# Optimization experiments

Hardware: AMD Instinct MI355X
Metric: run time of the kernel (lower is better)

The kernel has to match this reference:

```python
import jax, jax.numpy as jnp
import numpy as np

B, S, H, NH = 2, 2048, 1024, 16
HD = H // NH


def setup_inputs() -> dict:
    key = jax.random.key(0)
    ks = jax.random.split(key, 14)
    lim = 1.0 / np.sqrt(H)  # torch Linear default init range
    def lin(ka, kb):
        W = jax.random.uniform(ka, (H, H), jnp.float32, -lim, lim)
        b = jax.random.uniform(kb, (H,), jnp.float32, -lim, lim)
        return W, b
    Wq, bq = lin(ks[0], ks[1])
    Wk, bk = lin(ks[2], ks[3])
    Wv, bv = lin(ks[4], ks[5])
    Wo, bo = lin(ks[6], ks[7])
    return {
        "query": jax.random.normal(ks[8], (B, S, H), jnp.float32),
        "key": jax.random.normal(ks[9], (B, S, H), jnp.float32),
        "value": jax.random.normal(ks[10], (B, S, H), jnp.float32),
        "attn_mask": jax.random.randint(ks[11], (B, S, S), 0, 2).astype(bool),
        "relative_time": jax.random.normal(ks[12], (B, 1, S, S), jnp.float32),
        "Wq": Wq, "bq": bq, "Wk": Wk, "bk": bk,
        "Wv": Wv, "bv": bv, "Wo": Wo, "bo": bo,
    }


def reference(query, key, value, attn_mask, relative_time,
              Wq, bq, Wk, bk, Wv, bv, Wo, bo):
    Bq, Sq, _ = query.shape
    Skv = key.shape[1]
    # projections (torch Linear: x @ W^T + b)
    Q = (query @ Wq.T + bq).reshape(Bq, Sq, NH, HD).transpose(0, 2, 1, 3)
    K = (key @ Wk.T + bk).reshape(Bq, Skv, NH, HD).transpose(0, 2, 1, 3)
    V = (value @ Wv.T + bv).reshape(Bq, Skv, NH, HD).transpose(0, 2, 1, 3)
    scale = HD ** (-0.5)
    # NOTE: bias added BEFORE scaling, matching the original (non-standard)
    scores = jnp.einsum("bhqd,bhkd->bhqk", Q, K)
    scores = (scores + relative_time) * scale
    scores = jnp.where(attn_mask[:, None, :, :], scores, -jnp.inf)
    attn = jax.nn.softmax(scores.astype(jnp.float32), axis=-1).astype(scores.dtype)
    attn = jnp.nan_to_num(attn, nan=0.0)
    # dropout is identity in eval mode (dropout_rate applied only when training)
    out = jnp.einsum("bhqk,bhkd->bhqd", attn, V)
    out = out.transpose(0, 2, 1, 3).reshape(Bq, Sq, H)
    return out @ Wo.T + bo
```

## Files before the change

### kernel.cpp

```cpp
#include <hip/hip_runtime.h>
#include <hip/hip_bf16.h>

constexpr int BATCH = 2, SEQ = 2048, HDIM = 1024, NHEADS = 16, HEADD = 64;
constexpr int MROWS = BATCH * SEQ;
constexpr float QSCALE = 0.18033688011112042f;

typedef short short8  __attribute__((ext_vector_type(8)));
typedef float f32x4   __attribute__((ext_vector_type(4)));
typedef float f32x16  __attribute__((ext_vector_type(16)));
typedef int   int4v   __attribute__((ext_vector_type(4)));
typedef unsigned short ushort4v __attribute__((ext_vector_type(4)));

static __device__ __forceinline__ short f2bf(float f) {
    __hip_bfloat16 h = __float2bfloat16(f);
    return *reinterpret_cast<short*>(&h);
}

static __device__ __forceinline__ int cvt_pk_bf16(float a, float b) {
    int r;
    asm("v_cvt_pk_bf16_f32 %0, %1, %2" : "=v"(r) : "v"(a), "v"(b));
    return r;
}

static __device__ __forceinline__ float bfbits2f(unsigned short u) {
    return __builtin_bit_cast(float, (unsigned int)u << 16);
}

static __device__ __forceinline__ void gload_lds16(const void* g, void* l) {
    __builtin_amdgcn_global_load_lds(
        (const __attribute__((address_space(1))) unsigned int*)g,
        (__attribute__((address_space(3))) unsigned int*)l, 16, 0, 0);
}

__global__ void cvt_all_kernel(const float* __restrict__ q, const float* __restrict__ k,
                               const float* __restrict__ v, const float* __restrict__ w0,
                               const float* __restrict__ w1, const float* __restrict__ w2,
                               const float* __restrict__ w3,
                               short* __restrict__ xq, short* __restrict__ xk,
                               short* __restrict__ xv, short* __restrict__ o0,
                               short* __restrict__ o1, short* __restrict__ o2,
                               short* __restrict__ o3, int n4x, int n4w) {
    int i = blockIdx.x * blockDim.x + threadIdx.x;
    const int stride = gridDim.x * blockDim.x;
    const int total = 3 * n4x + 4 * n4w;
    for (; i < total; i += stride) {
        const float* in; short* out; int j = i;
        if (j < 3 * n4x) {
            if (j >= 2 * n4x)      { in = v; out = xv; j -= 2 * n4x; }
            else if (j >= n4x)     { in = k; out = xk; j -= n4x; }
            else                   { in = q; out = xq; }
        } else {
            j -= 3 * n4x;
            if (j >= 3 * n4w)      { in = w3; out = o3; j -= 3 * n4w; }
            else if (j >= 2 * n4w) { in = w2; out = o2; j -= 2 * n4w; }
            else if (j >= n4w)     { in = w1; out = o1; j -= n4w; }
            else                   { in = w0; out = o0; }
        }
        const float4 val = reinterpret_cast<const float4*>(in)[j];
        short4 o;
        o.x = f2bf(val.x); o.y = f2bf(val.y); o.z = f2bf(val.z); o.w = f2bf(val.w);
        reinterpret_cast<short4*>(out)[j] = o;
    }
}

__global__ void detect_mask_kernel(const unsigned int* __restrict__ m, int* flag) {
    const int tid = threadIdx.x;
    int gt1 = 0, isf = 0;
    for (int i = 0; i < 4; ++i) {
        unsigned int wv = m[tid + 256 * i];
        if (wv > 1u) gt1 = 1;
        if (wv == 0x3F800000u) isf = 1;
    }
    __shared__ int s_gt1, s_isf;
    if (tid == 0) { s_gt1 = 0; s_isf = 0; }
    __syncthreads();
    if (gt1) atomicOr(&s_gt1, 1);
    if (isf) atomicOr(&s_isf, 1);
    __syncthreads();
    if (tid == 0) flag[0] = s_gt1 ? (s_isf ? 2 : 1) : 0;
}

__global__ void fuse_rel_kernel(const float* __restrict__ rel, const void* __restrict__ mask,
                                const int* __restrict__ flag, short* __restrict__ rT,
                                int nThr) {
    const int f = flag[0];
    int i = blockIdx.x * blockDim.x + threadIdx.x;
    const int stride = gridDim.x * blockDim.x;
    for (; i < nThr; i += stride) {
        const int q    = i & 2047;
        const int kv16 = (i >> 11) & 127;
        const int b    = i >> 18;
        const long base = ((long)(b * 2048 + q)) * 2048 + kv16 * 16;
        float4 rv[4];
        #pragma unroll
        for (int g = 0; g < 4; ++g)
            rv[g] = *reinterpret_cast<const float4*>(rel + base + 4 * g);
        bool mk[16];
        if (f == 1) {
            const unsigned int* mp = (const unsigned int*)((const unsigned char*)mask + base);
            #pragma unroll
            for (int wd = 0; wd < 4; ++wd) {
                const unsigned int mw = mp[wd];
                #pragma unroll
                for (int s = 0; s < 4; ++s) mk[wd * 4 + s] = ((mw >> (8 * s)) & 0xffu) != 0;
            }
        } else if (f == 0) {
            const int* mp = (const int*)mask + base;
            #pragma unroll
            for (int j = 0; j < 16; ++j) mk[j] = mp[j] != 0;
        } else {
            const float* mp = (const float*)mask + base;
            #pragma unroll
            for (int j = 0; j < 16; ++j) mk[j] = mp[j] != 0.0f;
        }
        const float* rp = reinterpret_cast<const float*>(&rv[0]);
        #pragma unroll
        for (int g = 0; g < 4; ++g) {
            short4 o;
            short* op = reinterpret_cast<short*>(&o);
            #pragma unroll
            for (int j = 0; j < 4; ++j) {
                const int idx = 4 * g + j;
                op[j] = f2bf(mk[idx] ? rp[idx] * QSCALE : -1e30f);
            }
            *reinterpret_cast<short4*>(rT + (((long)(b * 512 + kv16 * 4 + g)) * 2048 + q) * 4) = o;
        }
    }
}

template<int BN, typename EPI>
static __device__ __forceinline__
void gemm_core(const short* A, const short* Bw, int K, int m0, int n0, EPI epi) {
    constexpr int NFRAG = BN / 32;
    __shared__ short As[128 * 64];
    __shared__ short Bs[BN * 64];
    const int tid  = threadIdx.x;
    const int lane = tid & 63;
    const int w    = tid >> 6;
    const int lo   = lane & 15, hi = lane >> 4;
    const int wm   = w >> 1, wn = w & 1;

    f32x4 acc[4][NFRAG] = {};

    const int arow = tid >> 3;
    const int acol = (tid & 7) * 8;
    const long aBase = (long)(m0 + arow) * K + acol;
    const long bBase = (long)(n0 + arow) * K + acol;

    for (int k0 = 0; k0 < K; k0 += 64) {
        #pragma unroll
        for (int i = 0; i < 4; ++i)
            gload_lds16(A + aBase + (long)i * 32 * K + k0, (char*)As + i * 4096 + tid * 16);
        #pragma unroll
        for (int i = 0; i < NFRAG; ++i)
            gload_lds16(Bw + bBase + (long)i * 32 * K + k0, (char*)Bs + i * 4096 + tid * 16);
        __syncthreads();
        #pragma unroll
        for (int ks = 0; ks < 2; ++ks) {
            short8 af[4], bf[NFRAG];
            const int koff = ks * 32 + hi * 8;
            #pragma unroll
            for (int fm = 0; fm < 4; ++fm)
                af[fm] = *reinterpret_cast<const short8*>(&As[(wm * 64 + fm * 16 + lo) * 64 + koff]);
            #pragma unroll
            for (int fn = 0; fn < NFRAG; ++fn)
                bf[fn] = *reinterpret_cast<const short8*>(&Bs[(wn * (BN / 2) + fn * 16 + lo) * 64 + koff]);
            #pragma unroll
            for (int fm = 0; fm < 4; ++fm)
                #pragma unroll
                for (int fn = 0; fn < NFRAG; ++fn)
                    acc[fm][fn] = __builtin_amdgcn_mfma_f32_16x16x32_bf16(
                        af[fm], bf[fn], acc[fm][fn], 0, 0, 0);
        }
        __syncthreads();
    }

    #pragma unroll
    for (int fm = 0; fm < 4; ++fm)
        #pragma unroll
        for (int fn = 0; fn < NFRAG; ++fn) {
            const int n = n0 + wn * (BN / 2) + fn * 16 + lo;
            const int mB = m0 + wm * 64 + fm * 16 + hi * 4;
            for (int r = 0; r < 4; ++r) epi(mB + r, n, acc[fm][fn][r]);
        }
}

__global__ __launch_bounds__(256, 2)
void qkv_gemm(const short* xq, const short* xk, const short* xv,
              const short* wq, const short* wk, const short* wv,
              const float* bq, const float* bk, const float* bv,
              short* Qb, short* Kb, short* Vt) {
    const int which = blockIdx.x >> 8;
    const int bid   = blockIdx.x & 255;
    const int m0 = (bid >> 3) << 7;
    const int n0 = (bid & 7) << 7;
    const short* A    = which == 0 ? xq : which == 1 ? xk : xv;
    const short* W    = which == 0 ? wq : which == 1 ? wk : wv;
    const float* bias = which == 0 ? bq : which == 1 ? bk : bv;
    short* C          = which == 0 ? Qb : which == 1 ? Kb : Vt;
    const float scale = which == 0 ? QSCALE : 1.0f;
    gemm_core<128>(A, W, HDIM, m0, n0, [&](int m, int n, float v) {
        v = (v + bias[n]) * scale;
        const int b = m >> 11, s = m & (SEQ - 1);
        const int h = n >> 6, d = n & 63;
        long idx;
        if (which != 2) idx = (((long)(b * NHEADS + h)) * SEQ + s) * HEADD + d;
        else            idx = (((long)(b * NHEADS + h)) * HEADD + d) * SEQ + s;
        C[idx] = f2bf(v);
    });
}

__global__ __launch_bounds__(256, 2)
void out_gemm(const short* A, const short* W, const float* bias, float* Cout) {
    const int bid = blockIdx.x;
    const int m0 = (bid >> 4) << 7;
    const int n0 = (bid & 15) << 6;
    gemm_core<64>(A, W, HDIM, m0, n0, [&](int m, int n, float v) {
        Cout[(long)m * HDIM + n] = v + bias[n];
    });
}

__global__ __launch_bounds__(256, 4)
void attn_fwd(const short* __restrict__ Qb, const short* __restrict__ Kb,
              const short* __restrict__ Vtb, const short* __restrict__ rT,
              short* __restrict__ Ob) {
    __shared__ short Ks[2][64 * 64];
    __shared__ short Vs[2][64 * 64];
    const int tid  = threadIdx.x;
    const int lane = tid & 63;
    const int wv   = tid >> 6;
    const int qp   = wv & 1;
    const int t    = wv >> 1;
    const int l31  = lane & 31, hi2 = lane >> 5;
    const int wg = ((blockIdx.x & 7) << 7) + (blockIdx.x >> 3);
    const int qt = wg & 31, h = (wg >> 5) & 15, b = wg >> 9;
    const int bh = b * NHEADS + h;
    const int q0 = qt * 64 + qp * 32 + l31;

    short8 qf[4];
    {
        const short* qp_ = Qb + ((long)bh * SEQ + q0) * HEADD + hi2 * 8;
        #pragma unroll
        for (int s = 0; s < 4; ++s)
            qf[s] = *reinterpret_cast<const short8*>(qp_ + s * 16);
    }

    float lsum = 0.0f;
    f32x16 oacc0 = {}, oacc1 = {};

    const int srow  = tid >> 3;
    const int scolb = (tid & 7) * 16;
    const int scolK = scolb ^ ((((srow & 7) ^ ((srow >> 3) & 3))) << 4);
    const char* KbB = (const char*)Kb + ((long)bh * SEQ + srow) * 128 + scolK;
    const char* VbB = (const char*)Vtb + ((long)bh * HEADD + srow) * ((long)SEQ * 2) + scolK;

    auto stage = [&](int buf, int kt) {
        #pragma unroll
        for (int i = 0; i < 2; ++i) {
            gload_lds16(KbB + ((long)kt * 64 + i * 32) * 128,
                        (char*)&Ks[buf][0] + i * 4096 + tid * 16);
            gload_lds16(VbB + (long)i * 32 * (SEQ * 2) + (long)kt * 128,
                        (char*)&Vs[buf][0] + i * 4096 + tid * 16);
        }
    };

    ushort4v rbuf[4];
    auto loadRel = [&](int kt) {
        #pragma unroll
        for (int g = 0; g < 4; ++g) {
            const int p4 = kt * 16 + t * 8 + 2 * g + hi2;
            rbuf[g] = *reinterpret_cast<const ushort4v*>(
                rT + (((long)(b * 512 + p4)) * 2048 + q0) * 4);
        }
    };

    stage(0, 0);
    loadRel(0);

    const int rsw = (((l31 & 7) ^ ((l31 >> 3) & 3))) << 4;
    const int NT = SEQ / 64;

    for (int kt = 0; kt < NT; ++kt) {
        const int cb = kt & 1;
        const bool hasNext = (kt < NT - 1);
        if (hasNext) stage(cb ^ 1, kt + 1);
        if (hasNext) asm volatile("s_waitcnt vmcnt(8)" ::: "memory");
        else         asm volatile("s_waitcnt vmcnt(4)" ::: "memory");
        __builtin_amdgcn_s_barrier();
        asm volatile("" ::: "memory");

        f32x16 sc;
        #pragma unroll
        for (int g = 0; g < 4; ++g)
            #pragma unroll
            for (int j = 0; j < 4; ++j)
                sc[4 * g + j] = bfbits2f(rbuf[g][j]);
        if (hasNext) loadRel(kt + 1);

        const char* kls = (const char*)&Ks[cb][0];
        const char* kr  = kls + (t * 32 + l31) * 128;
        __builtin_amdgcn_s_setprio(1);
        #pragma unroll
        for (int s = 0; s < 4; ++s) {
            short8 kf = *reinterpret_cast<const short8*>(kr + ((s * 32 + hi2 * 16) ^ rsw));
            sc = __builtin_amdgcn_mfma_f32_32x32x16_bf16(kf, qf[s], sc, 0, 0, 0);
        }
        __builtin_amdgcn_s_setprio(0);

        int X[8];
        #pragma unroll
        for (int i2 = 0; i2 < 8; ++i2) {
            const float p0 = __builtin_amdgcn_exp2f(sc[2 * i2]);
            const float p1 = __builtin_amdgcn_exp2f(sc[2 * i2 + 1]);
            lsum += p0 + p1;
            X[i2] = cvt_pk_bf16(p0, p1);
        }
        int pa[2][4];
        #pragma unroll
        for (int u = 0; u < 2; ++u) {
            auto r0 = __builtin_amdgcn_permlane32_swap(X[4 * u + 0], X[4 * u + 2], false, false);
            auto r1 = __builtin_amdgcn_permlane32_swap(X[4 * u + 1], X[4 * u + 3], false, false);
            pa[u][0] = (int)r0[0];
            pa[u][1] = (int)r1[0];
            pa[u][2] = (int)r0[1];
            pa[u][3] = (int)r1[1];
        }

        const char* vls = (const char*)&Vs[cb][0];
        __builtin_amdgcn_s_setprio(1);
        #pragma unroll
        for (int dt = 0; dt < 2; ++dt) {
            const char* vr = vls + (dt * 32 + l31) * 128;
            #pragma unroll
            for (int u = 0; u < 2; ++u) {
                const int s = 2 * t + u;
                short8 vf = *reinterpret_cast<const short8*>(vr + ((s * 32 + hi2 * 16) ^ rsw));
                int4v pw = { pa[u][0], pa[u][1], pa[u][2], pa[u][3] };
                if (dt == 0)
                    oacc0 = __builtin_amdgcn_mfma_f32_32x32x16_bf16(
                        __builtin_bit_cast(short8, pw), vf, oacc0, 0, 0, 0);
                else
                    oacc1 = __builtin_amdgcn_mfma_f32_32x32x16_bf16(
                        __builtin_bit_cast(short8, pw), vf, oacc1, 0, 0, 0);
            }
        }
        __builtin_amdgcn_s_setprio(0);

        asm volatile("" ::: "memory");
        __builtin_amdgcn_s_barrier();
    }

    lsum += __shfl_xor(lsum, 32, 64);

    float* cmbO = (float*)&Ks[0][0];
    float* cmbL = (float*)&Vs[0][0];
    if (t == 1) {
        #pragma unroll
        for (int r = 0; r < 16; ++r) {
            const int qloc = (r & 3) + 8 * (r >> 2) + 4 * hi2;
            cmbO[(qp * 32 + qloc) * 64 + l31]      = oacc0[r];
            cmbO[(qp * 32 + qloc) * 64 + 32 + l31] = oacc1[r];
        }
        if (hi2 == 0) cmbL[qp * 32 + l31] = lsum;
    }
    __syncthreads();
    if (t == 0) {
        const float ltot = lsum + cmbL[qp * 32 + l31];
        const float inv  = ltot > 0.0f ? 1.0f / ltot : 0.0f;
        #pragma unroll
        for (int r = 0; r < 16; ++r) {
            const int qloc = (r & 3) + 8 * (r >> 2) + 4 * hi2;
            const float invr = __shfl(inv, qloc, 64);
            const int qg = qt * 64 + qp * 32 + qloc;
            const long obase = ((long)b * SEQ + qg) * HDIM + h * 64 + l31;
            const float o0 = oacc0[r] + cmbO[(qp * 32 + qloc) * 64 + l31];
            const float o1 = oacc1[r] + cmbO[(qp * 32 + qloc) * 64 + 32 + l31];
            Ob[obase]      = f2bf(o0 * invr);
            Ob[obase + 32] = f2bf(o1 * invr);
        }
    }
}

extern "C" void kernel_launch(void* const* d_in, const int* in_sizes, int n_in,
                              void* d_out, int out_size, void* d_ws, size_t ws_size,
                              hipStream_t stream) {
    const float* q    = (const float*)d_in[0];
    const float* k    = (const float*)d_in[1];
    const float* v    = (const float*)d_in[2];
    const void*  mask = d_in[3];
    const float* rel  = (const float*)d_in[4];
    const float* Wq   = (const float*)d_in[5];
    const float* bq   = (const float*)d_in[6];
    const float* Wk   = (const float*)d_in[7];
    const float* bk   = (const float*)d_in[8];
    const float* Wv   = (const float*)d_in[9];
    const float* bv   = (const float*)d_in[10];
    const float* Wo   = (const float*)d_in[11];
    const float* bo   = (const float*)d_in[12];
    (void)in_sizes; (void)n_in; (void)out_size; (void)ws_size;

    char* ws = (char*)d_ws;
    size_t off = 0;
    auto alloc = [&](size_t bytes) {
        char* p = ws + off;
        off += (bytes + 255) & ~(size_t)255;
        return p;
    };
    const size_t xBytes = (size_t)MROWS * HDIM * 2;
    const size_t wBytes = (size_t)HDIM * HDIM * 2;
    const size_t poolBytes = 3 * xBytes + 3 * wBytes;

    short* Qb  = (short*)alloc(xBytes);
    short* Kb  = (short*)alloc(xBytes);
    short* Vt  = (short*)alloc(xBytes);
    short* wob = (short*)alloc(wBytes);
    int*   flag = (int*)alloc(256);
    char* pool = (char*)alloc(poolBytes);
    short* Ab  = (short*)alloc(xBytes);

    short* xq  = (short*)(pool);
    short* xk  = (short*)(pool + xBytes);
    short* xv  = (short*)(pool + 2 * xBytes);
    short* wqb = (short*)(pool + 3 * xBytes);
    short* wkb = (short*)(pool + 3 * xBytes + wBytes);
    short* wvb = (short*)(pool + 3 * xBytes + 2 * wBytes);
    short* rT  = (short*)(pool);

    const int n4x = MROWS * HDIM / 4, n4w = HDIM * HDIM / 4;
    cvt_all_kernel<<<2048, 256, 0, stream>>>(q, k, v, Wq, Wk, Wv, Wo,
                                             xq, xk, xv, wqb, wkb, wvb, wob, n4x, n4w);
    detect_mask_kernel<<<1, 256, 0, stream>>>((const unsigned int*)mask, flag);

    qkv_gemm<<<768, 256, 0, stream>>>(xq, xk, xv, wqb, wkb, wvb,
                                      bq, bk, bv, Qb, Kb, Vt);

    const int relThr = BATCH * 128 * 2048;
    fuse_rel_kernel<<<2048, 256, 0, stream>>>(rel, mask, flag, rT, relThr);

    attn_fwd<<<1024, 256, 0, stream>>>(Qb, Kb, Vt, rT, Ab);

    out_gemm<<<512, 256, 0, stream>>>(Ab, wob, bo, (float*)d_out);
}
```

Baseline: 162.7 us.

## Double-buffer the GEMM LDS tiles and tighten the attention vmcnt wait

The shared GEMM core now keeps two LDS buffers for A and B. It issues the global-to-LDS loads for the next K tile before computing on the current one, and needs one barrier per iteration instead of two. This is meant to hide global load latency behind the MFMA work in the projection GEMMs, at the cost of twice the LDS per block, which may limit occupancy. Separately, the attention loop's s_waitcnt vmcnt thresholds are lowered, so it waits for more outstanding loads. That looks like a correctness or ordering fix and may add stall time.

```diff
diff --git a/kernel.cpp b/kernel.cpp
--- a/kernel.cpp
+++ b/kernel.cpp
@@ -132,8 +132,8 @@
 static __device__ __forceinline__
 void gemm_core(const short* A, const short* Bw, int K, int m0, int n0, EPI epi) {
     constexpr int NFRAG = BN / 32;
-    __shared__ short As[128 * 64];
-    __shared__ short Bs[BN * 64];
+    __shared__ short As[2][128 * 64];
+    __shared__ short Bs[2][BN * 64];
     const int tid  = threadIdx.x;
     const int lane = tid & 63;
     const int w    = tid >> 6;
@@ -147,24 +147,35 @@
     const long aBase = (long)(m0 + arow) * K + acol;
     const long bBase = (long)(n0 + arow) * K + acol;
 
+    auto stage = [&](int buf, int k0) {
+        #pragma unroll
+        for (int i = 0; i < 4; ++i)
+            gload_lds16(A + aBase + (long)i * 32 * K + k0, (char*)&As[buf][0] + i * 4096 + tid * 16);
+        #pragma unroll
+        for (int i = 0; i < NFRAG; ++i)
+            gload_lds16(Bw + bBase + (long)i * 32 * K + k0, (char*)&Bs[buf][0] + i * 4096 + tid * 16);
+    };
+
+    stage(0, 0);
+    asm volatile("s_waitcnt vmcnt(0)" ::: "memory");
+    __builtin_amdgcn_s_barrier();
+    asm volatile("" ::: "memory");
+
+    int cur = 0;
     for (int k0 = 0; k0 < K; k0 += 64) {
-        #pragma unroll
-        for (int i = 0; i < 4; ++i)
-            gload_lds16(A + aBase + (long)i * 32 * K + k0, (char*)As + i * 4096 + tid * 16);
-        #pragma unroll
-        for (int i = 0; i < NFRAG; ++i)
-            gload_lds16(Bw + bBase + (long)i * 32 * K + k0, (char*)Bs + i * 4096 + tid * 16);
-        __syncthreads();
+        const bool hasNext = (k0 + 64 < K);
+        if (hasNext) stage(cur ^ 1, k0 + 64);
+
         #pragma unroll
         for (int ks = 0; ks < 2; ++ks) {
             short8 af[4], bf[NFRAG];
             const int koff = ks * 32 + hi * 8;
             #pragma unroll
             for (int fm = 0; fm < 4; ++fm)
-                af[fm] = *reinterpret_cast<const short8*>(&As[(wm * 64 + fm * 16 + lo) * 64 + koff]);
+                af[fm] = *reinterpret_cast<const short8*>(&As[cur][(wm * 64 + fm * 16 + lo) * 64 + koff]);
             #pragma unroll
             for (int fn = 0; fn < NFRAG; ++fn)
-                bf[fn] = *reinterpret_cast<const short8*>(&Bs[(wn * (BN / 2) + fn * 16 + lo) * 64 + koff]);
+                bf[fn] = *reinterpret_cast<const short8*>(&Bs[cur][(wn * (BN / 2) + fn * 16 + lo) * 64 + koff]);
             #pragma unroll
             for (int fm = 0; fm < 4; ++fm)
                 #pragma unroll
@@ -172,7 +183,14 @@
                     acc[fm][fn] = __builtin_amdgcn_mfma_f32_16x16x32_bf16(
                         af[fm], bf[fn], acc[fm][fn], 0, 0, 0);
         }
-        __syncthreads();
+
+        if (hasNext) {
+            asm volatile("" ::: "memory");
+            asm volatile("s_waitcnt vmcnt(0)" ::: "memory");
+            __builtin_amdgcn_s_barrier();
+            asm volatile("" ::: "memory");
+        }
+        cur ^= 1;
     }
 
     #pragma unroll
@@ -284,8 +302,8 @@
         const int cb = kt & 1;
         const bool hasNext = (kt < NT - 1);
         if (hasNext) stage(cb ^ 1, kt + 1);
-        if (hasNext) asm volatile("s_waitcnt vmcnt(8)" ::: "memory");
-        else         asm volatile("s_waitcnt vmcnt(4)" ::: "memory");
+        if (hasNext) asm volatile("s_waitcnt vmcnt(4)" ::: "memory");
+        else         asm volatile("s_waitcnt vmcnt(0)" ::: "memory");
         __builtin_amdgcn_s_barrier();
         asm volatile("" ::: "memory");
 
```

After: 181.5 us. +11.5%, slower.
